# Kernel tuning notes

Measured on AMD Instinct MI355X. Metric: run time of the kernel, lower is better.

Reference implementation:

```python
import jax, jax.numpy as jnp
import numpy as np

N_HEAD = 12
HEAD_DIM = 64
N_EMBD = 768
ATTN_MULT = 0.125
B, T = 2, 2048
NEG_INF = -1e30


def setup_inputs() -> dict:
    key = jax.random.key(0)
    ks = jax.random.split(key, 3)
    x = jax.random.normal(ks[0], (B, T, N_EMBD), dtype=jnp.float32)
    W_attn = jax.random.normal(ks[1], (N_EMBD, 3 * N_HEAD * HEAD_DIM), dtype=jnp.float32) * 0.02
    b_attn = jnp.zeros((3 * N_HEAD * HEAD_DIM,), dtype=jnp.float32)
    W_proj = jax.random.normal(ks[2], (N_HEAD * HEAD_DIM, N_EMBD), dtype=jnp.float32) * 0.02
    b_proj = jnp.zeros((N_EMBD,), dtype=jnp.float32)
    return {"x": x, "W_attn": W_attn, "b_attn": b_attn, "W_proj": W_proj, "b_proj": b_proj}


def reference(x, W_attn, b_attn, W_proj, b_proj):
    Bsz, Tlen, C = x.shape
    H, D = N_HEAD, HEAD_DIM
    qkv = x @ W_attn + b_attn                       # [B,T,3*H*D]
    q, k, v = jnp.split(qkv, 3, axis=-1)
    q = q.reshape(Bsz, Tlen, H, D).transpose(0, 2, 1, 3)   # [B,H,T,D]
    k = k.reshape(Bsz, Tlen, H, D).transpose(0, 2, 1, 3)
    v = v.reshape(Bsz, Tlen, H, D).transpose(0, 2, 1, 3)

    att = jnp.einsum('bhtd,bhsd->bhts', q, k) * ATTN_MULT  # [B,H,T,T]
    causal = jnp.tril(jnp.ones((Tlen, Tlen), dtype=bool))  # [T,T]
    att = jnp.where(causal, att, NEG_INF)

    # selection mask from head 0 (SelectionHeadLinearComboKind.NONE)
    S = jax.nn.relu(att[:, 0:1, :, :])                     # [B,1,T,T]; relu kills -inf
    # protect_bos_token: zero column 0 (key index 0)
    col = jnp.arange(Tlen)
    S = S * (col[None, None, None, :] != 0)
    # prevent_from_masking_myself: zero diagonal
    S = S * (1.0 - jnp.eye(Tlen, dtype=S.dtype))

    # accumulate selection over query (row) axis: ProtectionKind.NONE
    FF = jnp.cumsum(S, axis=-2)                            # [B,1,T,T]
    att = att - FF                                         # broadcast over heads

    p = jax.nn.softmax(att, axis=-1)                       # [B,H,T,T]
    y = jnp.einsum('bhts,bhsd->bhtd', p, v)                # [B,H,T,D]
    y = y.transpose(0, 2, 1, 3).reshape(Bsz, Tlen, H * D)  # [B,T,H*D]
    return y @ W_proj + b_proj
```

## Files before the change

kernel.cpp:

```cpp
#include <hip/hip_runtime.h>
#include <math.h>

#define T 2048
#define NH 12
#define HD 64
#define C3 2304
#define CE 768
#define NB 2

typedef __attribute__((ext_vector_type(8))) short bf16x8;
typedef __attribute__((ext_vector_type(4))) float f32x4;
typedef __attribute__((ext_vector_type(16))) float f32x16;
typedef __attribute__((ext_vector_type(4))) unsigned u32x4;

__device__ __forceinline__ void gload16(const void* g, void* l) {
    __builtin_amdgcn_global_load_lds(
        (const __attribute__((address_space(1))) void*)g,
        (__attribute__((address_space(3))) void*)l, 16, 0, 0);
}

__device__ inline void bf16split(float a, unsigned short& h, unsigned short& l) {
    unsigned int u = __float_as_uint(a);
    unsigned int r = (u + 0x7FFFu + ((u >> 16) & 1u)) >> 16;
    h = (unsigned short)r;
// ... 239 lines not shown
        #pragma unroll
        for (int fi = 0; fi < 4; ++fi)
            #pragma unroll
            for (int fj = 0; fj < 4; ++fj) {
                acc[fi][fj] = __builtin_amdgcn_mfma_f32_16x16x32_bf16(fb[0][fj], fa[0][fi], acc[fi][fj], 0, 0, 0);
                acc[fi][fj] = __builtin_amdgcn_mfma_f32_16x16x32_bf16(fb[0][fj], fa[1][fi], acc[fi][fj], 0, 0, 0);
                acc[fi][fj] = __builtin_amdgcn_mfma_f32_16x16x32_bf16(fb[1][fj], fa[0][fi], acc[fi][fj], 0, 0, 0);
            }
    }
    const int colbase = bn + wc * 64;
    const int region = colbase / 768;
    const int h = (colbase % 768) >> 6;
    const int mloc = lane & 15, ng = (lane >> 4) * 4;
    #pragma unroll
    for (int fi = 0; fi < 4; ++fi) {
        int tg = bm + wr * 64 + fi * 16 + mloc;
        int bb = tg >> 11, t = tg & (T - 1);
        #pragma unroll
        for (int fj = 0; fj < 4; ++fj) {
            int dbase = fj * 16 + ng;
            float4 bv = *reinterpret_cast<const float4*>(&bias[colbase + dbase]);
            float v0 = acc[fi][fj][0] + bv.x, v1 = acc[fi][fj][1] + bv.y;
            float v2 = acc[fi][fj][2] + bv.z, v3 = acc[fi][fj][3] + bv.w;
            size_t o = ((size_t)(bb * NH + h) * T + t) * 64 + dbase;
            if (region == 2) {
                float4 o4 = {v0, v1, v2, v3};
                *reinterpret_cast<float4*>(&Vtmp[o]) = o4;
            } else {
                unsigned short hh[4], ll[4];
                bf16split(v0, hh[0], ll[0]); bf16split(v1, hh[1], ll[1]);
                bf16split(v2, hh[2], ll[2]); bf16split(v3, hh[3], ll[3]);
                uint2 ph = {(unsigned)hh[0] | ((unsigned)hh[1] << 16),
                            (unsigned)hh[2] | ((unsigned)hh[3] << 16)};
                uint2 pl = {(unsigned)ll[0] | ((unsigned)ll[1] << 16),
                            (unsigned)ll[2] | ((unsigned)ll[3] << 16)};
                if (region == 0) {
                    *reinterpret_cast<uint2*>(&Qh[o]) = ph;
                    *reinterpret_cast<uint2*>(&Ql[o]) = pl;
                } else {
                    *reinterpret_cast<uint2*>(&Kh[o]) = ph;
                    *reinterpret_cast<uint2*>(&Kl[o]) = pl;
                }
            }
        }
    }
}

__global__ __launch_bounds__(256) void gemm_bias_kernel(
        const float* __restrict__ A, const float* __restrict__ B,
        const float* __restrict__ bias, float* __restrict__ Cm,
        int M, int N, int K) {
    __shared__ float As[16][64];
    __shared__ float Bs[16][68];
    const int tid = threadIdx.x;
    const int ty = tid >> 4, tx = tid & 15;
    const int bm = blockIdx.y * 64, bn = blockIdx.x * 64;
    float acc[4][4] = {};
    for (int k0 = 0; k0 < K; k0 += 16) {
        {
            int r = tid >> 2;
            int kk = (tid & 3) * 4;
            float4 a = *reinterpret_cast<const float4*>(&A[(size_t)(bm + r) * K + k0 + kk]);
            As[kk + 0][r] = a.x; As[kk + 1][r] = a.y; As[kk + 2][r] = a.z; As[kk + 3][r] = a.w;
        }
        {
            int kk = tid >> 4;
            int c = (tid & 15) * 4;
            *reinterpret_cast<float4*>(&Bs[kk][c]) =
                *reinterpret_cast<const float4*>(&B[(size_t)(k0 + kk) * N + bn + c]);
        }
        __syncthreads();
        #pragma unroll
        for (int kk = 0; kk < 16; ++kk) {
            float4 a4 = *reinterpret_cast<const float4*>(&As[kk][ty * 4]);
            float4 b4 = *reinterpret_cast<const float4*>(&Bs[kk][tx * 4]);
            float av[4] = {a4.x, a4.y, a4.z, a4.w};
            float bv[4] = {b4.x, b4.y, b4.z, b4.w};
            #pragma unroll
            for (int i = 0; i < 4; ++i)
                #pragma unroll
                for (int j = 0; j < 4; ++j)
                    acc[i][j] = fmaf(av[i], bv[j], acc[i][j]);
        }
        __syncthreads();
    }
    #pragma unroll
    for (int i = 0; i < 4; ++i) {
        int row = bm + ty * 4 + i;
        #pragma unroll
        for (int j = 0; j < 4; ++j) {
            int col = bn + tx * 4 + j;
            Cm[(size_t)row * N + col] = acc[i][j] + bias[col];
        }
    }
}

#define FST 72

__global__ __launch_bounds__(256) void s0_mfma_kernel(
        const unsigned short* __restrict__ Qh, const unsigned short* __restrict__ Ql,
        const unsigned short* __restrict__ Kh, const unsigned short* __restrict__ Kl,
        float* __restrict__ S, float* __restrict__ Psum) {
    const int kb = blockIdx.x * 64, qb = blockIdx.y * 64, b = blockIdx.z;
    const int tid = threadIdx.x;
    float* Sb = S + (size_t)b * T * T;
    if (kb > qb) {
        const int ty = tid >> 4, tx = tid & 15;
        #pragma unroll
        for (int i = 0; i < 4; ++i) {
            float4 z = {0.f, 0.f, 0.f, 0.f};
            *reinterpret_cast<float4*>(&Sb[(size_t)(qb + ty * 4 + i) * T + kb + tx * 4]) = z;
        }
        if (tid < 64) Psum[((size_t)(b * 32 + (qb >> 6)) * T) + kb + tid] = 0.f;
        return;
    }
    const int lane = tid & 63, w = tid >> 6;
    const int fr = lane & 15, fg = lane >> 4;
    __shared__ unsigned short Ks[2][64 * FST];
    __shared__ float csum[4][64];
    const int hb0 = b * NH;
    {
        const int sr = tid >> 2, sc0 = (tid & 3) * 16;
        const unsigned short* kh = Kh + ((size_t)hb0 * T + kb + sr) * 64 + sc0;
        const unsigned short* kl = Kl + ((size_t)hb0 * T + kb + sr) * 64 + sc0;
        uint4 a0 = reinterpret_cast<const uint4*>(kh)[0];
        uint4 a1 = reinterpret_cast<const uint4*>(kh)[1];
        uint4 b0 = reinterpret_cast<const uint4*>(kl)[0];
        uint4 b1 = reinterpret_cast<const uint4*>(kl)[1];
        *reinterpret_cast<uint4*>(&Ks[0][sr * FST + sc0 + 0]) = a0;
        *reinterpret_cast<uint4*>(&Ks[0][sr * FST + sc0 + 8]) = a1;
        *reinterpret_cast<uint4*>(&Ks[1][sr * FST + sc0 + 0]) = b0;
        *reinterpret_cast<uint4*>(&Ks[1][sr * FST + sc0 + 8]) = b1;
    }
    bf16x8 qh[2], ql[2];
    #pragma unroll
    for (int ks = 0; ks < 2; ++ks) {
        size_t qo = ((size_t)hb0 * T + qb + w * 16 + fr) * 64 + ks * 32 + fg * 8;
        qh[ks] = *reinterpret_cast<const bf16x8*>(&Qh[qo]);
        ql[ks] = *reinterpret_cast<const bf16x8*>(&Ql[qo]);
    }
    __syncthreads();
    f32x4 qk[4];
    #pragma unroll
    for (int fj = 0; fj < 4; ++fj) qk[fj] = (f32x4){0.f, 0.f, 0.f, 0.f};
    #pragma unroll
    for (int ks = 0; ks < 2; ++ks) {
        bf16x8 kbh[4], kbl[4];
        #pragma unroll
        for (int fj = 0; fj < 4; ++fj) {
            kbh[fj] = *reinterpret_cast<const bf16x8*>(&Ks[0][(fj * 16 + fr) * FST + ks * 32 + fg * 8]);
            kbl[fj] = *reinterpret_cast<const bf16x8*>(&Ks[1][(fj * 16 + fr) * FST + ks * 32 + fg * 8]);
        }
        #pragma unroll
        for (int fj = 0; fj < 4; ++fj) {
            qk[fj] = __builtin_amdgcn_mfma_f32_16x16x32_bf16(qh[ks], kbh[fj], qk[fj], 0, 0, 0);
            qk[fj] = __builtin_amdgcn_mfma_f32_16x16x32_bf16(qh[ks], kbl[fj], qk[fj], 0, 0, 0);
            qk[fj] = __builtin_amdgcn_mfma_f32_16x16x32_bf16(ql[ks], kbh[fj], qk[fj], 0, 0, 0);
        }
    }
    float colsum[4] = {0.f, 0.f, 0.f, 0.f};
    #pragma unroll
    for (int p = 0; p < 4; ++p) {
        int t = qb + w * 16 + fg * 4 + p;
        #pragma unroll
        for (int fj = 0; fj < 4; ++fj) {
            int s = kb + fj * 16 + fr;
            float v = qk[fj][p] * 0.125f;
            float o = (s >= 1 && s < t) ? fmaxf(v, 0.0f) : 0.0f;
            Sb[(size_t)t * T + s] = o;
            colsum[fj] += o;
        }
    }
    #pragma unroll
    for (int fj = 0; fj < 4; ++fj) {
        colsum[fj] += __shfl_xor(colsum[fj], 16);
        colsum[fj] += __shfl_xor(colsum[fj], 32);
    }
    if (lane < 16) {
        #pragma unroll
        for (int fj = 0; fj < 4; ++fj) csum[w][fj * 16 + lane] = colsum[fj];
    }
    __syncthreads();
    if (tid < 64) {
        float v = csum[0][tid] + csum[1][tid] + csum[2][tid] + csum[3][tid];
        Psum[((size_t)(b * 32 + (qb >> 6)) * T) + kb + tid] = v;
    }
}

__global__ __launch_bounds__(256) void s0_kernel(const float* __restrict__ qkv,
                                                 float* __restrict__ S) {
    const int kb = blockIdx.x * 64, qb = blockIdx.y * 64, b = blockIdx.z;
    const int tid = threadIdx.x, ty = tid >> 4, tx = tid & 15;
    float* Sb = S + (size_t)b * T * T;
    if (kb > qb) {
        #pragma unroll
        for (int i = 0; i < 4; ++i) {
            int row = qb + ty * 4 + i;
            float4 z = {0.f, 0.f, 0.f, 0.f};
            *reinterpret_cast<float4*>(&Sb[(size_t)row * T + kb + tx * 4]) = z;
        }
        return;
    }
    __shared__ float Qt[64][68];
    __shared__ float Kt[64][68];
    {
        int r = tid >> 2;
        int c0 = (tid & 3) * 16;
        const float* qrow = qkv + (size_t)(b * T + qb + r) * C3 + 0;
        const float* krow = qkv + (size_t)(b * T + kb + r) * C3 + 768;
        #pragma unroll
        for (int u = 0; u < 4; ++u) {
            float4 q4 = *reinterpret_cast<const float4*>(&qrow[c0 + u * 4]);
            float4 k4 = *reinterpret_cast<const float4*>(&krow[c0 + u * 4]);
            int d = c0 + u * 4;
            Qt[d + 0][r] = q4.x; Qt[d + 1][r] = q4.y; Qt[d + 2][r] = q4.z; Qt[d + 3][r] = q4.w;
            Kt[d + 0][r] = k4.x; Kt[d + 1][r] = k4.y; Kt[d + 2][r] = k4.z; Kt[d + 3][r] = k4.w;
        }
    }
    __syncthreads();
    float acc[4][4] = {};
    #pragma unroll
    for (int d = 0; d < 64; ++d) {
        float4 qv = *reinterpret_cast<const float4*>(&Qt[d][ty * 4]);
        float4 kv = *reinterpret_cast<const float4*>(&Kt[d][tx * 4]);
        float qa[4] = {qv.x, qv.y, qv.z, qv.w};
        float ka[4] = {kv.x, kv.y, kv.z, kv.w};
        #pragma unroll
        for (int i = 0; i < 4; ++i)
            #pragma unroll
            for (int j = 0; j < 4; ++j)
                acc[i][j] = fmaf(qa[i], ka[j], acc[i][j]);
    }
    #pragma unroll
    for (int i = 0; i < 4; ++i) {
        int t = qb + ty * 4 + i;
        float o[4];
        #pragma unroll
        for (int j = 0; j < 4; ++j) {
            int s = kb + tx * 4 + j;
            float v = acc[i][j] * 0.125f;
            o[j] = (s >= 1 && s < t) ? fmaxf(v, 0.0f) : 0.0f;
        }
        float4 o4 = {o[0], o[1], o[2], o[3]};
        *reinterpret_cast<float4*>(&Sb[(size_t)t * T + kb + tx * 4]) = o4;
    }
}

__global__ __launch_bounds__(256) void colsum_kernel(const float* __restrict__ S,
                                                     float* __restrict__ Psum) {
    int s = blockIdx.x * 256 + threadIdx.x;
    int j = blockIdx.y, b = blockIdx.z;
    const float* Sb = S + (size_t)b * T * T;
    float sum = 0.f;
    for (int r = 0; r < 64; ++r) sum += Sb[(size_t)(j * 64 + r) * T + s];
    Psum[((size_t)b * 32 + j) * T + s] = sum;
}

__global__ __launch_bounds__(256) void scanseg_kernel(float* __restrict__ Psum) {
    int s = blockIdx.x * 256 + threadIdx.x;
    int b = blockIdx.y;
    float v[32];
    #pragma unroll
    for (int j = 0; j < 32; ++j)
        v[j] = Psum[((size_t)(b * 32 + j)) * T + s];
    float run = 0.f;
    #pragma unroll
    for (int j = 0; j < 32; ++j) {
        Psum[((size_t)(b * 32 + j)) * T + s] = run;
        run += v[j];
    }
}

__global__ __launch_bounds__(256) void ffscan_kernel(float* __restrict__ S,
                                                     const float* __restrict__ Psum) {
    int s = blockIdx.x * 256 + threadIdx.x;
    int j = blockIdx.y, b = blockIdx.z;
    float run = Psum[((size_t)b * 32 + j) * T + s];
    float* Sb = S + (size_t)b * T * T;
    for (int r0 = 0; r0 < 64; r0 += 8) {
        float v[8];
        #pragma unroll
        for (int i = 0; i < 8; ++i)
            v[i] = Sb[(size_t)(j * 64 + r0 + i) * T + s];
        #pragma unroll
        for (int i = 0; i < 8; ++i) {
            run += v[i];
            Sb[(size_t)(j * 64 + r0 + i) * T + s] = run;
        }
    }
}

__device__ const int FTQ[40] = {15,15,15,15,14,14,14,13,13,13,12,12,12,11,11,11,10,10,9,9,8,8,7,7,6,5,4,3,14,10,6,2,13,9,5,1,12,8,4,0};
__device__ const int FK0[40] = {0,8,16,24,0,8,16,0,8,16,0,8,16,0,8,16,0,8,0,8,0,8,0,8,0,0,0,0,24,16,8,0,24,16,8,0,24,16,8,0};
__device__ const int FK1[40] = {8,16,24,32,8,16,24,8,16,24,8,16,24,8,16,24,8,16,8,16,8,16,8,16,8,8,8,8,30,22,14,6,28,20,12,4,26,18,10,2};
__device__ const int FCB[12] = {0,2,4,6,8,11,14,17,20,24,28,32};

__global__ __launch_bounds__(256) void flash_mfma_kernel(
        const unsigned short* __restrict__ Qh, const unsigned short* __restrict__ Ql,
        const unsigned short* __restrict__ Kh, const unsigned short* __restrict__ Kl,
        const unsigned short* __restrict__ Vth, const unsigned short* __restrict__ Vtl,
        const float* __restrict__ FF,
        unsigned short* __restrict__ Yh, unsigned short* __restrict__ Yl,
        float* __restrict__ PART) {
    const int hb = blockIdx.x;
    const int h = hb % NH, b = hb / NH;
    const int u = blockIdx.y;
    const int tq = FTQ[u], kt0 = FK0[u], kt1 = FK1[u];
    const int qb = tq * 128;
    const int tid = threadIdx.x;
    const int lane = tid & 63, w = tid >> 6;
    const int q31 = lane & 31, hi = lane >> 5;
    const int trow = qb + w * 32 + q31;
    __shared__ unsigned short KS[2][64 * FST];
    __shared__ unsigned short VS[2][64 * FST];

    bf16x8 qfh[4], qfl[4];
    #pragma unroll
    for (int dblk = 0; dblk < 4; ++dblk) {
        size_t qo = ((size_t)hb * T + trow) * 64 + dblk * 16 + hi * 8;
        qfh[dblk] = *reinterpret_cast<const bf16x8*>(&Qh[qo]);
        qfl[dblk] = *reinterpret_cast<const bf16x8*>(&Ql[qo]);
    }

    f32x16 oacc0 = (f32x16)(0.f), oacc1 = (f32x16)(0.f);
    float m = -1e30f, l = 0.f;
    const float* FFb = FF + (size_t)b * T * T;
    const int sr = tid >> 2, sc0 = (tid & 3) * 16;

    for (int kt = kt0; kt < kt1; ++kt) {
        const int kb = kt * 64;
        __syncthreads();
        {
            const unsigned short* ksrc = Kh + ((size_t)hb * T + kb + sr) * 64 + sc0;
            const unsigned short* ksrl = Kl + ((size_t)hb * T + kb + sr) * 64 + sc0;
            const unsigned short* vsrc = Vth + ((size_t)hb * 64 + sr) * T + kb + sc0;
            const unsigned short* vsrl = Vtl + ((size_t)hb * 64 + sr) * T + kb + sc0;
            uint4 k0v = reinterpret_cast<const uint4*>(ksrc)[0];
            uint4 k1v = reinterpret_cast<const uint4*>(ksrc)[1];
            uint4 k2v = reinterpret_cast<const uint4*>(ksrl)[0];
            uint4 k3v = reinterpret_cast<const uint4*>(ksrl)[1];
            uint4 v0v = reinterpret_cast<const uint4*>(vsrc)[0];
            uint4 v1v = reinterpret_cast<const uint4*>(vsrc)[1];
            uint4 v2v = reinterpret_cast<const uint4*>(vsrl)[0];
            uint4 v3v = reinterpret_cast<const uint4*>(vsrl)[1];
            *reinterpret_cast<uint4*>(&KS[0][sr * FST + sc0 + 0]) = k0v;
            *reinterpret_cast<uint4*>(&KS[0][sr * FST + sc0 + 8]) = k1v;
            *reinterpret_cast<uint4*>(&KS[1][sr * FST + sc0 + 0]) = k2v;
            *reinterpret_cast<uint4*>(&KS[1][sr * FST + sc0 + 8]) = k3v;
            *reinterpret_cast<uint4*>(&VS[0][sr * FST + sc0 + 0]) = v0v;
            *reinterpret_cast<uint4*>(&VS[0][sr * FST + sc0 + 8]) = v1v;
            *reinterpret_cast<uint4*>(&VS[1][sr * FST + sc0 + 0]) = v2v;
            *reinterpret_cast<uint4*>(&VS[1][sr * FST + sc0 + 8]) = v3v;
        }
        __syncthreads();
        f32x16 acc0 = (f32x16)(0.f), acc1 = (f32x16)(0.f);
        __builtin_amdgcn_s_setprio(1);
        #pragma unroll
        for (int dblk = 0; dblk < 4; ++dblk) {
            bf16x8 kfh = *reinterpret_cast<const bf16x8*>(&KS[0][(q31) * FST + dblk * 16 + hi * 8]);
            bf16x8 kfl = *reinterpret_cast<const bf16x8*>(&KS[1][(q31) * FST + dblk * 16 + hi * 8]);
            acc0 = __builtin_amdgcn_mfma_f32_32x32x16_bf16(kfh, qfh[dblk], acc0, 0, 0, 0);
            acc0 = __builtin_amdgcn_mfma_f32_32x32x16_bf16(kfh, qfl[dblk], acc0, 0, 0, 0);
            acc0 = __builtin_amdgcn_mfma_f32_32x32x16_bf16(kfl, qfh[dblk], acc0, 0, 0, 0);
        }
        __builtin_amdgcn_s_setprio(0);
        float4 ffv[2][4];
        #pragma unroll
        for (int sb = 0; sb < 2; ++sb)
            #pragma unroll
            for (int g = 0; g < 4; ++g)
                ffv[sb][g] = *reinterpret_cast<const float4*>(
                    &FFb[(size_t)trow * T + kb + sb * 32 + g * 8 + hi * 4]);
        __builtin_amdgcn_s_setprio(1);
        #pragma unroll
        for (int dblk = 0; dblk < 4; ++dblk) {
            bf16x8 kfh = *reinterpret_cast<const bf16x8*>(&KS[0][(32 + q31) * FST + dblk * 16 + hi * 8]);
            bf16x8 kfl = *reinterpret_cast<const bf16x8*>(&KS[1][(32 + q31) * FST + dblk * 16 + hi * 8]);
            acc1 = __builtin_amdgcn_mfma_f32_32x32x16_bf16(kfh, qfh[dblk], acc1, 0, 0, 0);
            acc1 = __builtin_amdgcn_mfma_f32_32x32x16_bf16(kfh, qfl[dblk], acc1, 0, 0, 0);
            acc1 = __builtin_amdgcn_mfma_f32_32x32x16_bf16(kfl, qfh[dblk], acc1, 0, 0, 0);
        }
        __builtin_amdgcn_s_setprio(0);
        float pv[2][16];
        #pragma unroll
        for (int g = 0; g < 4; ++g) {
            float fv0[4] = {ffv[0][g].x, ffv[0][g].y, ffv[0][g].z, ffv[0][g].w};
            float fv1[4] = {ffv[1][g].x, ffv[1][g].y, ffv[1][g].z, ffv[1][g].w};
            #pragma unroll
            for (int a = 0; a < 4; ++a) {
                int r = g * 4 + a;
                int s0i = kb + a + g * 8 + hi * 4;
                int s1i = s0i + 32;
                float v0 = acc0[r] * 0.125f - fv0[a];
                float v1 = acc1[r] * 0.125f - fv1[a];
                pv[0][r] = (s0i <= trow) ? v0 : -1e30f;
                pv[1][r] = (s1i <= trow) ? v1 : -1e30f;
            }
        }
        float tm = pv[0][0];
        #pragma unroll
        for (int sb = 0; sb < 2; ++sb)
            #pragma unroll
            for (int r = 0; r < 16; ++r) tm = fmaxf(tm, pv[sb][r]);
        tm = fmaxf(tm, __shfl_xor(tm, 32));
        float mn = fmaxf(m, tm);
        float scale = __expf(m - mn);
        float rs = 0.f;
        #pragma unroll
        for (int sb = 0; sb < 2; ++sb)
            #pragma unroll
            for (int r = 0; r < 16; ++r) {
                float pe = __expf(pv[sb][r] - mn);
                pv[sb][r] = pe; rs += pe;
            }
        rs += __shfl_xor(rs, 32);
        l = l * scale + rs;
        m = mn;
        oacc0 *= scale; oacc1 *= scale;
        unsigned wh[2][4][2], wl[2][4][2];
        #pragma unroll
        for (int sb = 0; sb < 2; ++sb)
            #pragma unroll
            for (int bq = 0; bq < 4; ++bq)
                #pragma unroll
                for (int h2 = 0; h2 < 2; ++h2)
                    packPfast(pv[sb][4 * bq + 2 * h2], pv[sb][4 * bq + 2 * h2 + 1],
                              wh[sb][bq][h2], wl[sb][bq][h2]);
        #pragma unroll
        for (int kk = 0; kk < 4; ++kk) {
            const int sb = kk >> 1;
            const int b0 = 2 * (kk & 1), b1 = b0 + 1;
            unsigned sh_b1_0 = (unsigned)__shfl_xor((int)wh[sb][b1][0], 32);
            unsigned sh_b1_1 = (unsigned)__shfl_xor((int)wh[sb][b1][1], 32);
            unsigned sh_b0_0 = (unsigned)__shfl_xor((int)wh[sb][b0][0], 32);
            unsigned sh_b0_1 = (unsigned)__shfl_xor((int)wh[sb][b0][1], 32);
            unsigned sl_b1_0 = (unsigned)__shfl_xor((int)wl[sb][b1][0], 32);
            unsigned sl_b1_1 = (unsigned)__shfl_xor((int)wl[sb][b1][1], 32);
            unsigned sl_b0_0 = (unsigned)__shfl_xor((int)wl[sb][b0][0], 32);
            unsigned sl_b0_1 = (unsigned)__shfl_xor((int)wl[sb][b0][1], 32);
            u32x4 th, tl;
            th[0] = hi ? sh_b1_0 : wh[sb][b0][0];
            th[1] = hi ? sh_b1_1 : wh[sb][b0][1];
            th[2] = hi ? wh[sb][b1][0] : sh_b0_0;
            th[3] = hi ? wh[sb][b1][1] : sh_b0_1;
            tl[0] = hi ? sl_b1_0 : wl[sb][b0][0];
            tl[1] = hi ? sl_b1_1 : wl[sb][b0][1];
            tl[2] = hi ? wl[sb][b1][0] : sl_b0_0;
            tl[3] = hi ? wl[sb][b1][1] : sl_b0_1;
            bf16x8 pbh = __builtin_bit_cast(bf16x8, th);
            bf16x8 pbl = __builtin_bit_cast(bf16x8, tl);
            {
                bf16x8 vfh = *reinterpret_cast<const bf16x8*>(&VS[0][(q31) * FST + kk * 16 + hi * 8]);
                bf16x8 vfl = *reinterpret_cast<const bf16x8*>(&VS[1][(q31) * FST + kk * 16 + hi * 8]);
                __builtin_amdgcn_s_setprio(1);
                oacc0 = __builtin_amdgcn_mfma_f32_32x32x16_bf16(vfh, pbh, oacc0, 0, 0, 0);
                oacc0 = __builtin_amdgcn_mfma_f32_32x32x16_bf16(vfh, pbl, oacc0, 0, 0, 0);
                oacc0 = __builtin_amdgcn_mfma_f32_32x32x16_bf16(vfl, pbh, oacc0, 0, 0, 0);
                __builtin_amdgcn_s_setprio(0);
            }
            {
                bf16x8 vfh = *reinterpret_cast<const bf16x8*>(&VS[0][(32 + q31) * FST + kk * 16 + hi * 8]);
                bf16x8 vfl = *reinterpret_cast<const bf16x8*>(&VS[1][(32 + q31) * FST + kk * 16 + hi * 8]);
                __builtin_amdgcn_s_setprio(1);
                oacc1 = __builtin_amdgcn_mfma_f32_32x32x16_bf16(vfh, pbh, oacc1, 0, 0, 0);
                oacc1 = __builtin_amdgcn_mfma_f32_32x32x16_bf16(vfh, pbl, oacc1, 0, 0, 0);
                oacc1 = __builtin_amdgcn_mfma_f32_32x32x16_bf16(vfl, pbh, oacc1, 0, 0, 0);
                __builtin_amdgcn_s_setprio(0);
            }
        }
    }
    if (tq < 4) {
        float inv = 1.f / l;
        size_t ybase = ((size_t)(b * T + trow)) * CE + h * 64;
        #pragma unroll
        for (int g = 0; g < 4; ++g) {
            unsigned short h0[4], l0[4], h1[4], l1[4];
            #pragma unroll
            for (int i = 0; i < 4; ++i) {
                bf16split(oacc0[4 * g + i] * inv, h0[i], l0[i]);
                bf16split(oacc1[4 * g + i] * inv, h1[i], l1[i]);
            }
            uint2 ph0 = {(unsigned)h0[0] | ((unsigned)h0[1] << 16), (unsigned)h0[2] | ((unsigned)h0[3] << 16)};
            uint2 pl0 = {(unsigned)l0[0] | ((unsigned)l0[1] << 16), (unsigned)l0[2] | ((unsigned)l0[3] << 16)};
            uint2 ph1 = {(unsigned)h1[0] | ((unsigned)h1[1] << 16), (unsigned)h1[2] | ((unsigned)h1[3] << 16)};
            uint2 pl1 = {(unsigned)l1[0] | ((unsigned)l1[1] << 16), (unsigned)l1[2] | ((unsigned)l1[3] << 16)};
            *reinterpret_cast<uint2*>(&Yh[ybase + g * 8 + hi * 4]) = ph0;
            *reinterpret_cast<uint2*>(&Yl[ybase + g * 8 + hi * 4]) = pl0;
            *reinterpret_cast<uint2*>(&Yh[ybase + 32 + g * 8 + hi * 4]) = ph1;
            *reinterpret_cast<uint2*>(&Yl[ybase + 32 + g * 8 + hi * 4]) = pl1;
        }
    } else {
        const int ci = FCB[tq - 4] + (kt0 >> 3);
        float* Ob = PART + (size_t)(hb * 36 + ci) * 8448;
        const int rr = w * 32 + q31;
        #pragma unroll
        for (int g = 0; g < 4; ++g) {
            float4 o0 = {oacc0[4 * g + 0], oacc0[4 * g + 1], oacc0[4 * g + 2], oacc0[4 * g + 3]};
            float4 o1 = {oacc1[4 * g + 0], oacc1[4 * g + 1], oacc1[4 * g + 2], oacc1[4 * g + 3]};
            *reinterpret_cast<float4*>(&Ob[rr * 64 + g * 8 + hi * 4]) = o0;
            *reinterpret_cast<float4*>(&Ob[rr * 64 + 32 + g * 8 + hi * 4]) = o1;
        }
        if (hi == 0) { Ob[8192 + rr] = m; Ob[8192 + 128 + rr] = l; }
    }
}

__global__ __launch_bounds__(256) void merge128_kernel(const float* __restrict__ PART,
                                                       unsigned short* __restrict__ Yh,
                                                       unsigned short* __restrict__ Yl) {
    const int hb = blockIdx.x;
    const int tq = 4 + blockIdx.y;
    const int h = hb % NH, b = hb / NH;
    const int nch = (tq >= 12) ? 4 : (tq >= 8) ? 3 : 2;
    const float* base = PART + (size_t)(hb * 36 + FCB[tq - 4]) * 8448;
    const int tid = threadIdx.x;
    const int r = tid >> 1, half = tid & 1;
    float mm[4], la[4];
    float M = -1e30f;
    #pragma unroll
    for (int c = 0; c < 4; ++c) {
        int cc = (c < nch) ? c : 0;
        float mv = base[(size_t)cc * 8448 + 8192 + r];
        float lv = base[(size_t)cc * 8448 + 8192 + 128 + r];
        mm[c] = (c < nch) ? mv : -1e30f;
        la[c] = (c < nch) ? lv : 0.f;
        M = fmaxf(M, mm[c]);
    }
    float a[4], L = 0.f;
    #pragma unroll
    for (int c = 0; c < 4; ++c) {
        a[c] = (c < nch) ? __expf(mm[c] - M) : 0.f;
        L += a[c] * la[c];
    }
    float inv = 1.f / L;
    const int t = tq * 128 + r;
    size_t ybase = ((size_t)(b * T + t)) * CE + h * 64 + half * 32;
    #pragma unroll
    for (int uu = 0; uu < 8; ++uu) {
        float ax = 0.f, ay = 0.f, az = 0.f, aw = 0.f;
        #pragma unroll
        for (int c = 0; c < 4; ++c) {
            int cc = (c < nch) ? c : 0;
            float4 x = *reinterpret_cast<const float4*>(
                &base[(size_t)cc * 8448 + r * 64 + half * 32 + uu * 4]);
            ax += a[c] * x.x; ay += a[c] * x.y; az += a[c] * x.z; aw += a[c] * x.w;
        }
        unsigned short hh[4], ll[4];
        bf16split(ax * inv, hh[0], ll[0]); bf16split(ay * inv, hh[1], ll[1]);
        bf16split(az * inv, hh[2], ll[2]); bf16split(aw * inv, hh[3], ll[3]);
        uint2 ph = {(unsigned)hh[0] | ((unsigned)hh[1] << 16), (unsigned)hh[2] | ((unsigned)hh[3] << 16)};
        uint2 pl = {(unsigned)ll[0] | ((unsigned)ll[1] << 16), (unsigned)ll[2] | ((unsigned)ll[3] << 16)};
        *reinterpret_cast<uint2*>(&Yh[ybase + uu * 4]) = ph;
        *reinterpret_cast<uint2*>(&Yl[ybase + uu * 4]) = pl;
    }
}

__global__ __launch_bounds__(256) void flash_kernel(const float* __restrict__ qkv,
                                                    const float* __restrict__ FF,
                                                    float* __restrict__ Y,
                                                    float* __restrict__ PO,
                                                    float* __restrict__ PML,
                                                    int split) {
    const int hb = blockIdx.x;
    const int h = hb % NH, b = hb / NH;
    int qt, kt0, kt1, mode;
    if (split) {
        const int u = blockIdx.y;
        if (u < 16)      { qt = 16 + u; kt0 = 0;  kt1 = 16;     mode = 1; }
        else if (u < 32) { qt = 31 - u; kt0 = 0;  kt1 = qt + 1; mode = 0; }
        else             { qt = 63 - u; kt0 = 16; kt1 = qt + 1; mode = 2; }
    } else {
        qt = 31 - blockIdx.y; kt0 = 0; kt1 = qt + 1; mode = 0;
    }
    const int qb = qt * 64;
    const int tid = threadIdx.x, ty = tid >> 4, tx = tid & 15;
    __shared__ float Qt[64][68];
    __shared__ float KtPs[64][68];
    __shared__ float Vs[64][68];
    const int r = tid >> 2, c0 = (tid & 3) * 16;
    {
        const float* qrow = qkv + (size_t)(b * T + qb + r) * C3 + h * 64;
        #pragma unroll
        for (int u = 0; u < 4; ++u) {
            float4 q4 = *reinterpret_cast<const float4*>(&qrow[c0 + u * 4]);
            int d = c0 + u * 4;
            Qt[d + 0][r] = q4.x; Qt[d + 1][r] = q4.y; Qt[d + 2][r] = q4.z; Qt[d + 3][r] = q4.w;
        }
    }
    float m[4], l[4], O[4][4];
    #pragma unroll
    for (int i = 0; i < 4; ++i) {
        m[i] = -1e30f; l[i] = 0.f;
        #pragma unroll
        for (int j = 0; j < 4; ++j) O[i][j] = 0.f;
    }
    const float* FFb = FF + (size_t)b * T * T;
    for (int kt = kt0; kt < kt1; ++kt) {
        const int kb = kt * 64;
        __syncthreads();
        {
            const float* krow = qkv + (size_t)(b * T + kb + r) * C3 + 768 + h * 64;
            const float* vrow = qkv + (size_t)(b * T + kb + r) * C3 + 1536 + h * 64;
            #pragma unroll
            for (int u = 0; u < 4; ++u) {
                float4 k4 = *reinterpret_cast<const float4*>(&krow[c0 + u * 4]);
                int d = c0 + u * 4;
                KtPs[d + 0][r] = k4.x; KtPs[d + 1][r] = k4.y;
                KtPs[d + 2][r] = k4.z; KtPs[d + 3][r] = k4.w;
                *reinterpret_cast<float4*>(&Vs[r][c0 + u * 4]) =
                    *reinterpret_cast<const float4*>(&vrow[c0 + u * 4]);
            }
        }
        __syncthreads();
        float sc[4][4] = {};
        #pragma unroll
        for (int d = 0; d < 64; ++d) {
            float4 qv = *reinterpret_cast<const float4*>(&Qt[d][ty * 4]);
            float4 kv = *reinterpret_cast<const float4*>(&KtPs[d][tx * 4]);
            float qa[4] = {qv.x, qv.y, qv.z, qv.w};
            float ka[4] = {kv.x, kv.y, kv.z, kv.w};
            #pragma unroll
            for (int i = 0; i < 4; ++i)
                #pragma unroll
                for (int j = 0; j < 4; ++j)
                    sc[i][j] = fmaf(qa[i], ka[j], sc[i][j]);
        }
        #pragma unroll
        for (int i = 0; i < 4; ++i) {
            int t = qb + ty * 4 + i;
            float4 f4 = *reinterpret_cast<const float4*>(&FFb[(size_t)t * T + kb + tx * 4]);
            float fv[4] = {f4.x, f4.y, f4.z, f4.w};
            #pragma unroll
            for (int j = 0; j < 4; ++j) {
                int s = kb + tx * 4 + j;
                float v = sc[i][j] * 0.125f - fv[j];
                sc[i][j] = (s <= t) ? v : -1e30f;
            }
        }
        #pragma unroll
        for (int i = 0; i < 4; ++i) {
            float tm = fmaxf(fmaxf(sc[i][0], sc[i][1]), fmaxf(sc[i][2], sc[i][3]));
            tm = fmaxf(tm, __shfl_xor(tm, 1));
            tm = fmaxf(tm, __shfl_xor(tm, 2));
            tm = fmaxf(tm, __shfl_xor(tm, 4));
            tm = fmaxf(tm, __shfl_xor(tm, 8));
            float mn = fmaxf(m[i], tm);
            float scale = __expf(m[i] - mn);
            float rs = 0.f;
            #pragma unroll
            for (int j = 0; j < 4; ++j) {
                float p = __expf(sc[i][j] - mn);
                sc[i][j] = p; rs += p;
            }
            rs += __shfl_xor(rs, 1); rs += __shfl_xor(rs, 2);
            rs += __shfl_xor(rs, 4); rs += __shfl_xor(rs, 8);
            l[i] = l[i] * scale + rs;
            m[i] = mn;
            #pragma unroll
            for (int j = 0; j < 4; ++j) O[i][j] *= scale;
        }
        __syncthreads();
        #pragma unroll
        for (int i = 0; i < 4; ++i) {
            float4 p4 = {sc[i][0], sc[i][1], sc[i][2], sc[i][3]};
            *reinterpret_cast<float4*>(&KtPs[ty * 4 + i][tx * 4]) = p4;
        }
        __syncthreads();
        #pragma unroll
        for (int j4 = 0; j4 < 16; ++j4) {
            float pvv[4][4];
            #pragma unroll
            for (int i = 0; i < 4; ++i) {
                float4 t4 = *reinterpret_cast<const float4*>(&KtPs[ty * 4 + i][j4 * 4]);
                pvv[i][0] = t4.x; pvv[i][1] = t4.y; pvv[i][2] = t4.z; pvv[i][3] = t4.w;
            }
            #pragma unroll
            for (int jj = 0; jj < 4; ++jj) {
                float4 v4 = *reinterpret_cast<const float4*>(&Vs[j4 * 4 + jj][tx * 4]);
                float vv[4] = {v4.x, v4.y, v4.z, v4.w};
                #pragma unroll
                for (int i = 0; i < 4; ++i)
                    #pragma unroll
                    for (int dd = 0; dd < 4; ++dd)
                        O[i][dd] = fmaf(pvv[i][jj], vv[dd], O[i][dd]);
            }
        }
    }
    if (mode == 0) {
        #pragma unroll
        for (int i = 0; i < 4; ++i) {
            int t = qb + ty * 4 + i;
            float inv = 1.f / l[i];
            float4 o4 = {O[i][0] * inv, O[i][1] * inv, O[i][2] * inv, O[i][3] * inv};
            *reinterpret_cast<float4*>(&Y[(size_t)(b * T + t) * CE + h * 64 + tx * 4]) = o4;
        }
    } else {
        const int pidx = (b * NH + h) * 16 + (qt - 16);
        float* Ob  = PO  + (size_t)(mode - 1) * (NB * NH * 16 * 4096) + (size_t)pidx * 4096;
        float* mlb = PML + (size_t)(mode - 1) * (NB * NH * 16 * 128)  + (size_t)pidx * 128;
        #pragma unroll
        for (int i = 0; i < 4; ++i) {
            int rr = ty * 4 + i;
            float4 o4 = {O[i][0], O[i][1], O[i][2], O[i][3]};
            *reinterpret_cast<float4*>(&Ob[rr * 64 + tx * 4]) = o4;
            if (tx == 0) { mlb[rr] = m[i]; mlb[64 + rr] = l[i]; }
        }
    }
}

__global__ __launch_bounds__(256) void merge_kernel(const float* __restrict__ PO,
                                                    const float* __restrict__ PML,
                                                    float* __restrict__ Y) {
    const int p = blockIdx.x;
    const int q16 = p & 15;
    const int hb = p >> 4;
    const int h = hb % NH, b = hb / NH;
    const int qt = 16 + q16;
    const float* O0  = PO  + (size_t)p * 4096;
    const float* O1  = PO  + (size_t)(NB * NH * 16) * 4096 + (size_t)p * 4096;
    const float* ml0 = PML + (size_t)p * 128;
    const float* ml1 = PML + (size_t)(NB * NH * 16) * 128  + (size_t)p * 128;
    const int tid = threadIdx.x;
    const int r = tid >> 2, c0 = (tid & 3) * 16;
    float m0 = ml0[r], l0 = ml0[64 + r];
    float m1 = ml1[r], l1 = ml1[64 + r];
    float M  = fmaxf(m0, m1);
    float a0 = __expf(m0 - M), a1 = __expf(m1 - M);
    float inv = 1.f / (a0 * l0 + a1 * l1);
    const int t = qt * 64 + r;
    float* Yrow = Y + (size_t)(b * T + t) * CE + h * 64;
    #pragma unroll
    for (int u = 0; u < 4; ++u) {
        float4 x0 = *reinterpret_cast<const float4*>(&O0[r * 64 + c0 + u * 4]);
        float4 x1 = *reinterpret_cast<const float4*>(&O1[r * 64 + c0 + u * 4]);
        float4 y;
        y.x = (a0 * x0.x + a1 * x1.x) * inv;
        y.y = (a0 * x0.y + a1 * x1.y) * inv;
        y.z = (a0 * x0.z + a1 * x1.z) * inv;
        y.w = (a0 * x0.w + a1 * x1.w) * inv;
        *reinterpret_cast<float4*>(&Yrow[c0 + u * 4]) = y;
    }
}

extern "C" void kernel_launch(void* const* d_in, const int* in_sizes, int n_in,
                              void* d_out, int out_size, void* d_ws, size_t ws_size,
                              hipStream_t stream) {
    const float* x      = (const float*)d_in[0];
    const float* W_attn = (const float*)d_in[1];
    const float* b_attn = (const float*)d_in[2];
    const float* W_proj = (const float*)d_in[3];
    const float* b_proj = (const float*)d_in[4];
    float* out = (float*)d_out;

    char* ws = (char*)d_ws;
    const size_t QKV_BYTES = (size_t)NB * T * C3 * 4;
    const size_t S_BYTES   = (size_t)NB * T * T * 4;
    const size_t P_BYTES   = (size_t)NB * 32 * T * 4;
    const size_t Y_BYTES   = (size_t)NB * T * CE * 4;
    const size_t PO_BYTES  = (size_t)2 * NB * NH * 16 * 4096 * 4;
    const size_t PML_BYTES = (size_t)2 * NB * NH * 16 * 128 * 4;
    const size_t PLANE_X   = (size_t)NB * T * CE * 2;
    const size_t PLANE_WA  = (size_t)C3 * CE * 2;
    const size_t PLANE_WP  = (size_t)CE * CE * 2;
    const size_t PLANE_KV  = (size_t)NB * NH * T * 64 * 2;

    const size_t U_OFF  = QKV_BYTES + S_BYTES + P_BYTES + Y_BYTES;
    const size_t U_SIZE = PO_BYTES + PML_BYTES;
    const size_t W_OFF  = U_OFF + U_SIZE;
    const size_t KV_OFF = W_OFF + 2 * PLANE_WA + 2 * PLANE_WP;

    float* qkv  = (float*)ws;
    float* Vtmp = (float*)ws;
    float* PART = (float*)ws;
    float* S    = (float*)(ws + QKV_BYTES);
    float* Psum = (float*)(ws + QKV_BYTES + S_BYTES);
    float* Yb   = (float*)(ws + QKV_BYTES + S_BYTES + P_BYTES);
    unsigned short* Qhp = (unsigned short*)(ws + QKV_BYTES + S_BYTES + P_BYTES);
    unsigned short* Qlp = (unsigned short*)(ws + QKV_BYTES + S_BYTES + P_BYTES + PLANE_X);
    float* PO   = (float*)(ws + U_OFF);
    float* PML  = (float*)(ws + U_OFF + PO_BYTES);
    unsigned short* Xh  = (unsigned short*)(ws + U_OFF);
    unsigned short* Xl  = (unsigned short*)(ws + U_OFF + PLANE_X);
    unsigned short* Yhp = Xh;
    unsigned short* Ylp = Xl;
    unsigned short* WAh = (unsigned short*)(ws + W_OFF);
    unsigned short* WAl = (unsigned short*)(ws + W_OFF + PLANE_WA);
    unsigned short* WPh = (unsigned short*)(ws + W_OFF + 2 * PLANE_WA);
    unsigned short* WPl = (unsigned short*)(ws + W_OFF + 2 * PLANE_WA + PLANE_WP);
    unsigned short* Khp = (unsigned short*)(ws + KV_OFF);
    unsigned short* Klp = (unsigned short*)(ws + KV_OFF + PLANE_KV);
    unsigned short* VTh = (unsigned short*)(ws + KV_OFF + 2 * PLANE_KV);
    unsigned short* VTl = (unsigned short*)(ws + KV_OFF + 3 * PLANE_KV);

    const size_t NEED_SPLIT = U_OFF + U_SIZE;
    const size_t NEED_MFMA  = KV_OFF;
    const size_t NEED_KV    = KV_OFF + 4 * PLANE_KV;
    const int split = (ws_size >= NEED_SPLIT) ? 1 : 0;
    const int mfma  = (ws_size >= NEED_MFMA) ? 1 : 0;
    const int kv    = (ws_size >= NEED_KV && mfma) ? 1 : 0;

    const int M = NB * T;

    if (kv) {
        cvt_split_T_kernel<<<dim3(C3 / 64, CE / 64), 256, 0, stream>>>(W_attn, WAh, WAl, CE, C3);
// ... 42 lines not shown
```

Before: 247.4 us.

## Prefetch next K/V tile into registers and remap blocks across XCDs

```diff
diff --git a/kernel.cpp b/kernel.cpp
--- a/kernel.cpp
+++ b/kernel.cpp
@@ -565,9 +565,10 @@
         const float* __restrict__ FF,
         unsigned short* __restrict__ Yh, unsigned short* __restrict__ Yl,
         float* __restrict__ PART) {
-    const int hb = blockIdx.x;
+    int g = blockIdx.y * gridDim.x + blockIdx.x;
+    const int hb = (g & 7) * 3 + ((g >> 3) % 3);
+    const int u  = (g >> 3) / 3;
     const int h = hb % NH, b = hb / NH;
-    const int u = blockIdx.y;
     const int tq = FTQ[u], kt0 = FK0[u], kt1 = FK1[u];
     const int qb = tq * 128;
     const int tid = threadIdx.x;
@@ -590,34 +591,51 @@
     const float* FFb = FF + (size_t)b * T * T;
     const int sr = tid >> 2, sc0 = (tid & 3) * 16;
 
+    {
+        const int kb = kt0 * 64;
+        const unsigned short* ksrc = Kh + ((size_t)hb * T + kb + sr) * 64 + sc0;
+        const unsigned short* ksrl = Kl + ((size_t)hb * T + kb + sr) * 64 + sc0;
+        const unsigned short* vsrc = Vth + ((size_t)hb * 64 + sr) * T + kb + sc0;
+        const unsigned short* vsrl = Vtl + ((size_t)hb * 64 + sr) * T + kb + sc0;
+        uint4 a0 = reinterpret_cast<const uint4*>(ksrc)[0];
+        uint4 a1 = reinterpret_cast<const uint4*>(ksrc)[1];
+        uint4 a2 = reinterpret_cast<const uint4*>(ksrl)[0];
+        uint4 a3 = reinterpret_cast<const uint4*>(ksrl)[1];
+        uint4 a4 = reinterpret_cast<const uint4*>(vsrc)[0];
+        uint4 a5 = reinterpret_cast<const uint4*>(vsrc)[1];
+        uint4 a6 = reinterpret_cast<const uint4*>(vsrl)[0];
+        uint4 a7 = reinterpret_cast<const uint4*>(vsrl)[1];
+        *reinterpret_cast<uint4*>(&KS[0][sr * FST + sc0 + 0]) = a0;
+        *reinterpret_cast<uint4*>(&KS[0][sr * FST + sc0 + 8]) = a1;
+        *reinterpret_cast<uint4*>(&KS[1][sr * FST + sc0 + 0]) = a2;
+        *reinterpret_cast<uint4*>(&KS[1][sr * FST + sc0 + 8]) = a3;
+        *reinterpret_cast<uint4*>(&VS[0][sr * FST + sc0 + 0]) = a4;
+        *reinterpret_cast<uint4*>(&VS[0][sr * FST + sc0 + 8]) = a5;
+        *reinterpret_cast<uint4*>(&VS[1][sr * FST + sc0 + 0]) = a6;
+        *reinterpret_cast<uint4*>(&VS[1][sr * FST + sc0 + 8]) = a7;
+    }
+    __syncthreads();
+
     for (int kt = kt0; kt < kt1; ++kt) {
         const int kb = kt * 64;
-        __syncthreads();
-        {
-            const unsigned short* ksrc = Kh + ((size_t)hb * T + kb + sr) * 64 + sc0;
-            const unsigned short* ksrl = Kl + ((size_t)hb * T + kb + sr) * 64 + sc0;
-            const unsigned short* vsrc = Vth + ((size_t)hb * 64 + sr) * T + kb + sc0;
-            const unsigned short* vsrl = Vtl + ((size_t)hb * 64 + sr) * T + kb + sc0;
-            uint4 k0v = reinterpret_cast<const uint4*>(ksrc)[0];
-            uint4 k1v = reinterpret_cast<const uint4*>(ksrc)[1];
-            uint4 k2v = reinterpret_cast<const uint4*>(ksrl)[0];
-            uint4 k3v = reinterpret_cast<const uint4*>(ksrl)[1];
-            uint4 v0v = reinterpret_cast<const uint4*>(vsrc)[0];
-            uint4 v1v = reinterpret_cast<const uint4*>(vsrc)[1];
-            uint4 v2v = reinterpret_cast<const uint4*>(vsrl)[0];
-            uint4 v3v = reinterpret_cast<const uint4*>(vsrl)[1];
-            *reinterpret_cast<uint4*>(&KS[0][sr * FST + sc0 + 0]) = k0v;
-            *reinterpret_cast<uint4*>(&KS[0][sr * FST + sc0 + 8]) = k1v;
-            *reinterpret_cast<uint4*>(&KS[1][sr * FST + sc0 + 0]) = k2v;
-            *reinterpret_cast<uint4*>(&KS[1][sr * FST + sc0 + 8]) = k3v;
-            *reinterpret_cast<uint4*>(&VS[0][sr * FST + sc0 + 0]) = v0v;
-            *reinterpret_cast<uint4*>(&VS[0][sr * FST + sc0 + 8]) = v1v;
-            *reinterpret_cast<uint4*>(&VS[1][sr * FST + sc0 + 0]) = v2v;
-            *reinterpret_cast<uint4*>(&VS[1][sr * FST + sc0 + 8]) = v3v;
-        }
-        __syncthreads();
+        const bool has_next = (kt + 1 < kt1);
+        uint4 p0, p1, p2, p3, p4, p5, p6, p7;
+        if (has_next) {
+            const int kb2 = kb + 64;
+            const unsigned short* ksrc = Kh + ((size_t)hb * T + kb2 + sr) * 64 + sc0;
+            const unsigned short* ksrl = Kl + ((size_t)hb * T + kb2 + sr) * 64 + sc0;
+            const unsigned short* vsrc = Vth + ((size_t)hb * 64 + sr) * T + kb2 + sc0;
+            const unsigned short* vsrl = Vtl + ((size_t)hb * 64 + sr) * T + kb2 + sc0;
+            p0 = reinterpret_cast<const uint4*>(ksrc)[0];
+            p1 = reinterpret_cast<const uint4*>(ksrc)[1];
+            p2 = reinterpret_cast<const uint4*>(ksrl)[0];
+            p3 = reinterpret_cast<const uint4*>(ksrl)[1];
+            p4 = reinterpret_cast<const uint4*>(vsrc)[0];
+            p5 = reinterpret_cast<const uint4*>(vsrc)[1];
+            p6 = reinterpret_cast<const uint4*>(vsrl)[0];
+            p7 = reinterpret_cast<const uint4*>(vsrl)[1];
+        }
         f32x16 acc0 = (f32x16)(0.f), acc1 = (f32x16)(0.f);
-        __builtin_amdgcn_s_setprio(1);
         #pragma unroll
         for (int dblk = 0; dblk < 4; ++dblk) {
             bf16x8 kfh = *reinterpret_cast<const bf16x8*>(&KS[0][(q31) * FST + dblk * 16 + hi * 8]);
@@ -626,15 +644,13 @@
             acc0 = __builtin_amdgcn_mfma_f32_32x32x16_bf16(kfh, qfl[dblk], acc0, 0, 0, 0);
             acc0 = __builtin_amdgcn_mfma_f32_32x32x16_bf16(kfl, qfh[dblk], acc0, 0, 0, 0);
         }
-        __builtin_amdgcn_s_setprio(0);
         float4 ffv[2][4];
         #pragma unroll
         for (int sb = 0; sb < 2; ++sb)
             #pragma unroll
-            for (int g = 0; g < 4; ++g)
-                ffv[sb][g] = *reinterpret_cast<const float4*>(
-                    &FFb[(size_t)trow * T + kb + sb * 32 + g * 8 + hi * 4]);
-        __builtin_amdgcn_s_setprio(1);
+            for (int gg = 0; gg < 4; ++gg)
+                ffv[sb][gg] = *reinterpret_cast<const float4*>(
+                    &FFb[(size_t)trow * T + kb + sb * 32 + gg * 8 + hi * 4]);
         #pragma unroll
         for (int dblk = 0; dblk < 4; ++dblk) {
             bf16x8 kfh = *reinterpret_cast<const bf16x8*>(&KS[0][(32 + q31) * FST + dblk * 16 + hi * 8]);
@@ -643,16 +659,15 @@
             acc1 = __builtin_amdgcn_mfma_f32_32x32x16_bf16(kfh, qfl[dblk], acc1, 0, 0, 0);
             acc1 = __builtin_amdgcn_mfma_f32_32x32x16_bf16(kfl, qfh[dblk], acc1, 0, 0, 0);
         }
-        __builtin_amdgcn_s_setprio(0);
         float pv[2][16];
         #pragma unroll
-        for (int g = 0; g < 4; ++g) {
-            float fv0[4] = {ffv[0][g].x, ffv[0][g].y, ffv[0][g].z, ffv[0][g].w};
-            float fv1[4] = {ffv[1][g].x, ffv[1][g].y, ffv[1][g].z, ffv[1][g].w};
+        for (int gg = 0; gg < 4; ++gg) {
+            float fv0[4] = {ffv[0][gg].x, ffv[0][gg].y, ffv[0][gg].z, ffv[0][gg].w};
+            float fv1[4] = {ffv[1][gg].x, ffv[1][gg].y, ffv[1][gg].z, ffv[1][gg].w};
             #pragma unroll
             for (int a = 0; a < 4; ++a) {
-                int r = g * 4 + a;
-                int s0i = kb + a + g * 8 + hi * 4;
+                int r = gg * 4 + a;
+                int s0i = kb + a + gg * 8 + hi * 4;
                 int s1i = s0i + 32;
                 float v0 = acc0[r] * 0.125f - fv0[a];
                 float v1 = acc1[r] * 0.125f - fv1[a];
@@ -715,53 +730,61 @@
             {
                 bf16x8 vfh = *reinterpret_cast<const bf16x8*>(&VS[0][(q31) * FST + kk * 16 + hi * 8]);
                 bf16x8 vfl = *reinterpret_cast<const bf16x8*>(&VS[1][(q31) * FST + kk * 16 + hi * 8]);
-                __builtin_amdgcn_s_setprio(1);
                 oacc0 = __builtin_amdgcn_mfma_f32_32x32x16_bf16(vfh, pbh, oacc0, 0, 0, 0);
                 oacc0 = __builtin_amdgcn_mfma_f32_32x32x16_bf16(vfh, pbl, oacc0, 0, 0, 0);
                 oacc0 = __builtin_amdgcn_mfma_f32_32x32x16_bf16(vfl, pbh, oacc0, 0, 0, 0);
-                __builtin_amdgcn_s_setprio(0);
             }
             {
                 bf16x8 vfh = *reinterpret_cast<const bf16x8*>(&VS[0][(32 + q31) * FST + kk * 16 + hi * 8]);
                 bf16x8 vfl = *reinterpret_cast<const bf16x8*>(&VS[1][(32 + q31) * FST + kk * 16 + hi * 8]);
-                __builtin_amdgcn_s_setprio(1);
                 oacc1 = __builtin_amdgcn_mfma_f32_32x32x16_bf16(vfh, pbh, oacc1, 0, 0, 0);
                 oacc1 = __builtin_amdgcn_mfma_f32_32x32x16_bf16(vfh, pbl, oacc1, 0, 0, 0);
                 oacc1 = __builtin_amdgcn_mfma_f32_32x32x16_bf16(vfl, pbh, oacc1, 0, 0, 0);
-                __builtin_amdgcn_s_setprio(0);
-            }
-        }
+            }
+        }
+        __syncthreads();
+        if (has_next) {
+            *reinterpret_cast<uint4*>(&KS[0][sr * FST + sc0 + 0]) = p0;
+            *reinterpret_cast<uint4*>(&KS[0][sr * FST + sc0 + 8]) = p1;
+            *reinterpret_cast<uint4*>(&KS[1][sr * FST + sc0 + 0]) = p2;
+            *reinterpret_cast<uint4*>(&KS[1][sr * FST + sc0 + 8]) = p3;
+            *reinterpret_cast<uint4*>(&VS[0][sr * FST + sc0 + 0]) = p4;
+            *reinterpret_cast<uint4*>(&VS[0][sr * FST + sc0 + 8]) = p5;
+            *reinterpret_cast<uint4*>(&VS[1][sr * FST + sc0 + 0]) = p6;
+            *reinterpret_cast<uint4*>(&VS[1][sr * FST + sc0 + 8]) = p7;
+        }
+        __syncthreads();
     }
     if (tq < 4) {
         float inv = 1.f / l;
         size_t ybase = ((size_t)(b * T + trow)) * CE + h * 64;
         #pragma unroll
-        for (int g = 0; g < 4; ++g) {
+        for (int gg = 0; gg < 4; ++gg) {
             unsigned short h0[4], l0[4], h1[4], l1[4];
             #pragma unroll
             for (int i = 0; i < 4; ++i) {
-                bf16split(oacc0[4 * g + i] * inv, h0[i], l0[i]);
-                bf16split(oacc1[4 * g + i] * inv, h1[i], l1[i]);
+                bf16split(oacc0[4 * gg + i] * inv, h0[i], l0[i]);
+                bf16split(oacc1[4 * gg + i] * inv, h1[i], l1[i]);
             }
             uint2 ph0 = {(unsigned)h0[0] | ((unsigned)h0[1] << 16), (unsigned)h0[2] | ((unsigned)h0[3] << 16)};
             uint2 pl0 = {(unsigned)l0[0] | ((unsigned)l0[1] << 16), (unsigned)l0[2] | ((unsigned)l0[3] << 16)};
             uint2 ph1 = {(unsigned)h1[0] | ((unsigned)h1[1] << 16), (unsigned)h1[2] | ((unsigned)h1[3] << 16)};
             uint2 pl1 = {(unsigned)l1[0] | ((unsigned)l1[1] << 16), (unsigned)l1[2] | ((unsigned)l1[3] << 16)};
-            *reinterpret_cast<uint2*>(&Yh[ybase + g * 8 + hi * 4]) = ph0;
-            *reinterpret_cast<uint2*>(&Yl[ybase + g * 8 + hi * 4]) = pl0;
-            *reinterpret_cast<uint2*>(&Yh[ybase + 32 + g * 8 + hi * 4]) = ph1;
-            *reinterpret_cast<uint2*>(&Yl[ybase + 32 + g * 8 + hi * 4]) = pl1;
+            *reinterpret_cast<uint2*>(&Yh[ybase + gg * 8 + hi * 4]) = ph0;
+            *reinterpret_cast<uint2*>(&Yl[ybase + gg * 8 + hi * 4]) = pl0;
+            *reinterpret_cast<uint2*>(&Yh[ybase + 32 + gg * 8 + hi * 4]) = ph1;
+            *reinterpret_cast<uint2*>(&Yl[ybase + 32 + gg * 8 + hi * 4]) = pl1;
         }
     } else {
         const int ci = FCB[tq - 4] + (kt0 >> 3);
         float* Ob = PART + (size_t)(hb * 36 + ci) * 8448;
         const int rr = w * 32 + q31;
         #pragma unroll
-        for (int g = 0; g < 4; ++g) {
-            float4 o0 = {oacc0[4 * g + 0], oacc0[4 * g + 1], oacc0[4 * g + 2], oacc0[4 * g + 3]};
-            float4 o1 = {oacc1[4 * g + 0], oacc1[4 * g + 1], oacc1[4 * g + 2], oacc1[4 * g + 3]};
-            *reinterpret_cast<float4*>(&Ob[rr * 64 + g * 8 + hi * 4]) = o0;
-            *reinterpret_cast<float4*>(&Ob[rr * 64 + 32 + g * 8 + hi * 4]) = o1;
+        for (int gg = 0; gg < 4; ++gg) {
+            float4 o0 = {oacc0[4 * gg + 0], oacc0[4 * gg + 1], oacc0[4 * gg + 2], oacc0[4 * gg + 3]};
+            float4 o1 = {oacc1[4 * gg + 0], oacc1[4 * gg + 1], oacc1[4 * gg + 2], oacc1[4 * gg + 3]};
+            *reinterpret_cast<float4*>(&Ob[rr * 64 + gg * 8 + hi * 4]) = o0;
+            *reinterpret_cast<float4*>(&Ob[rr * 64 + 32 + gg * 8 + hi * 4]) = o1;
         }
         if (hi == 0) { Ob[8192 + rr] = m; Ob[8192 + 128 + rr] = l; }
     }
```

After: 247.3 us, median of 2. About the same (-0.0%).
